# Kernel tuning notes

Measured on AMD Instinct MI355X. Metric: run time of the kernel, lower is better.

## Reference

```python
import jax, jax.numpy as jnp
import numpy as np

TOPK = 13
NUM_CLASSES = 80
ALPHA = 1.0
BETA = 6.0
EPS = 1e-9
B, N, IMG = 16, 100, 640


def _anchor_points():
    pts = []
    for s in (8, 16, 32):
        n = IMG // s
        xs = (jnp.arange(n, dtype=jnp.float32) + 0.5) * s
        gy, gx = jnp.meshgrid(xs, xs, indexing='ij')
        pts.append(jnp.stack([gx.reshape(-1), gy.reshape(-1)], axis=-1))
    return jnp.concatenate(pts, axis=0)  # [8400, 2]


def setup_inputs() -> dict:
    key = jax.random.key(0)
    k = jax.random.split(key, 6)
    anchor_points = _anchor_points()
    M = anchor_points.shape[0]
    pred_scores = jax.random.uniform(k[0], (B, M, NUM_CLASSES), dtype=jnp.float32)
    ctr = anchor_points[None] + jax.random.normal(k[1], (B, M, 2), dtype=jnp.float32) * 8.0
    wh = jax.random.uniform(k[2], (B, M, 2), minval=8.0, maxval=128.0, dtype=jnp.float32)
    pred_bboxes = jnp.concatenate([ctr - wh * 0.5, ctr + wh * 0.5], axis=-1)
    gctr = jax.random.uniform(k[3], (B, N, 2), minval=32.0, maxval=IMG - 32.0, dtype=jnp.float32)
    gwh = jax.random.uniform(k[4], (B, N, 2), minval=16.0, maxval=256.0, dtype=jnp.float32)
    gt_bboxes = jnp.concatenate([gctr - gwh * 0.5, gctr + gwh * 0.5], axis=-1)
    gt_labels = jax.random.randint(k[5], (B, N, 1), 0, NUM_CLASSES)
    # first 60 GTs valid per image
    mask_gt = (jnp.arange(N)[None, :, None] < 60).astype(jnp.float32) * jnp.ones((B, 1, 1), jnp.float32)
    return dict(pred_scores=pred_scores, pred_bboxes=pred_bboxes, anchor_points=anchor_points,
                gt_bboxes=gt_bboxes, gt_labels=gt_labels, mask_gt=mask_gt)


def _iou(gt, pr):
    # gt [B,N,4], pr [B,M,4] -> [B,N,M]
    gt = gt[:, :, None, :]
    pr = pr[:, None, :, :]
    lt = jnp.maximum(gt[..., :2], pr[..., :2])
    rb = jnp.minimum(gt[..., 2:], pr[..., 2:])
    wh = jnp.clip(rb - lt, 0.0)
    inter = wh[..., 0] * wh[..., 1]
    ag = (gt[..., 2] - gt[..., 0]) * (gt[..., 3] - gt[..., 1])
    ap = (pr[..., 2] - pr[..., 0]) * (pr[..., 3] - pr[..., 1])
    return jnp.clip(inter / (ag + ap - inter + EPS), 0.0)


def _forward(pred_scores, pred_bboxes, anchor_points, gt_bboxes, gt_labels, mask_gt):
    Bq, M, C = pred_scores.shape
    Nq = gt_bboxes.shape[1]
    lab = gt_labels[..., 0].astype(jnp.int32)  # [B,N]
    # gather class score of each GT's label at every anchor: [B,N,M]
    cls = jnp.take_along_axis(pred_scores.transpose(0, 2, 1), lab[:, :, None], axis=1)
    overlaps = _iou(gt_bboxes, pred_bboxes)                       # [B,N,M]
    align = (cls ** ALPHA) * (overlaps ** BETA)                   # [B,N,M]
    # anchor-center-in-gt mask
    ap = anchor_points[None, None, :, :]                          # [1,1,M,2]
    d = jnp.concatenate([ap - gt_bboxes[:, :, None, :2], gt_bboxes[:, :, None, 2:] - ap], axis=-1)
    in_gts = (jnp.min(d, axis=-1) > EPS).astype(align.dtype)      # [B,N,M]
    # top-k candidates per GT
    _, idx = jax.lax.top_k(align * in_gts, TOPK)                  # [B,N,K]
    tmask = jnp.broadcast_to(mask_gt.astype(bool), (Bq, Nq, TOPK))
    idx = jnp.where(tmask, idx, 0)
    bi = jnp.arange(Bq)[:, None, None]
    ni = jnp.arange(Nq)[None, :, None]
    cnt = jnp.zeros((Bq, Nq, M), align.dtype).at[bi, ni, idx].add(1.0)
    is_in_topk = jnp.where(cnt > 1, jnp.zeros_like(cnt), cnt)
    mask_pos = is_in_topk * in_gts * mask_gt                      # [B,N,M]
    # resolve anchors assigned to multiple GTs by highest IoU
    fg = mask_pos.sum(axis=-2)                                    # [B,M]
    multi = fg[:, None, :] > 1
    max_idx = jnp.argmax(overlaps, axis=1)                        # [B,M]
    is_max = (jnp.arange(Nq)[None, :, None] == max_idx[:, None, :]).astype(mask_pos.dtype)
    mask_pos = jnp.where(multi, is_max, mask_pos)
    fg = mask_pos.sum(axis=-2)
    tgt_idx = jnp.argmax(mask_pos, axis=-2)                       # [B,M]
    # assemble targets
    tl = jnp.take_along_axis(lab, tgt_idx, axis=1)                # [B,M]
    tb = jnp.take_along_axis(gt_bboxes, tgt_idx[..., None], axis=1)  # [B,M,4]
    tl = jnp.where(fg > 0, tl, NUM_CLASSES)                       # bg index for negatives
    ts = jax.nn.one_hot(tl, NUM_CLASSES + 1, dtype=pred_scores.dtype)[..., :NUM_CLASSES]
    # normalized align metric scaling
    am = align * mask_pos
    pa = am.max(axis=-1, keepdims=True)                           # [B,N,1]
    po = (overlaps * mask_pos).max(axis=-1, keepdims=True)        # [B,N,1]
    norm = (am * po / (pa + EPS)).max(axis=-2)[..., None]         # [B,M,1]
    ts = ts * norm
    return tl, tb, ts, fg > 0


def reference(pred_scores, pred_bboxes, anchor_points, gt_bboxes, gt_labels, mask_gt):
    return _forward(pred_scores, pred_bboxes, anchor_points, gt_bboxes, gt_labels, mask_gt)
```

## Files before the change

### kernel.cpp

```cpp
#include <hip/hip_runtime.h>

#define BB 16
#define NN 100
#define MM 8400
#define CC 80
#define TOPK 13
#define EPSF 1e-9f

#define OUT_TL 0
#define OUT_TB (BB*MM)
#define OUT_TS (OUT_TB + BB*MM*4)
#define OUT_FG (OUT_TS + BB*MM*CC)

__device__ __forceinline__ float iou_f(float gx1, float gy1, float gx2, float gy2,
                                       float px1, float py1, float px2, float py2) {
    float ltx = fmaxf(gx1, px1), lty = fmaxf(gy1, py1);
    float rbx = fminf(gx2, px2), rby = fminf(gy2, py2);
    float w = fmaxf(rbx - ltx, 0.0f), h = fmaxf(rby - lty, 0.0f);
    float inter = w * h;
    float ag  = (gx2 - gx1) * (gy2 - gy1);
    float ap_ = (px2 - px1) * (py2 - py1);
    float r = inter / (ag + ap_ - inter + EPSF);
    return fmaxf(r, 0.0f);
}

__global__ __launch_bounds__(256) void k_init(float* __restrict__ out,
                                              int* __restrict__ fg_cnt,
                                              int* __restrict__ sel_n,
                                              unsigned* __restrict__ pa,
                                              unsigned* __restrict__ po) {
    int i = blockIdx.x * blockDim.x + threadIdx.x;
    int stride = gridDim.x * blockDim.x;
    float4* ts4 = (float4*)(out + OUT_TS);
    const int nts4 = BB * MM * CC / 4;
    float4 z = make_float4(0.f, 0.f, 0.f, 0.f);
    for (int j = i; j < nts4; j += stride) ts4[j] = z;
    for (int j = i; j < BB * MM; j += stride) { fg_cnt[j] = 0; sel_n[j] = 0x7fffffff; }
    for (int j = i; j < BB * NN; j += stride) { pa[j] = 0u; po[j] = 0u; }
}

__global__ __launch_bounds__(256) void k_topk(const float* __restrict__ ps,
                                              const float* __restrict__ pb,
                                              const float* __restrict__ ap,
                                              const float* __restrict__ gtb,
                                              const int* __restrict__ lab,
                                              const float* __restrict__ mgt,
                                              int* __restrict__ fg_cnt,
                                              int* __restrict__ sel_n) {
    int row = blockIdx.x;
    int b = row / NN;
    int n = row - b * NN;
    int tid = threadIdx.x;

    __shared__ float swV[4];
    __shared__ int   swI[4];

    if (mgt[row] == 0.0f) return;

    float gx1 = gtb[row * 4 + 0], gy1 = gtb[row * 4 + 1];
    float gx2 = gtb[row * 4 + 2], gy2 = gtb[row * 4 + 3];
    int l = lab[row];
    const float* psb = ps + (size_t)b * MM * CC + l;
    const float* pbb = pb + (size_t)b * MM * 4;

    float v[33];
    unsigned long long insideMask = 0ull;
    float lmax = -1.0f; int lidx = MM;

#pragma unroll
    for (int j = 0; j < 33; ++j) {
        int m = tid + (j << 8);
        bool valid = (j < 32) || (tid < 208);
        int mc = valid ? m : (MM - 1);
        float ax = ap[2 * mc], ay = ap[2 * mc + 1];
        float dmin = fminf(fminf(ax - gx1, ay - gy1), fminf(gx2 - ax, gy2 - ay));
        bool inside = valid && (dmin > EPSF);
        float val = valid ? 0.0f : -1.0f;
        if (__any(inside)) {
            if (inside) {
                float4 p = *(const float4*)(pbb + (size_t)m * 4);
                float ov = iou_f(gx1, gy1, gx2, gy2, p.x, p.y, p.z, p.w);
                float cls = psb[(size_t)m * CC];
                float o2 = ov * ov;
                val = cls * (o2 * o2 * o2);
                insideMask |= (1ull << j);
            }
        }
        v[j] = val;
        if (val > lmax) { lmax = val; lidx = m; }
    }

    for (int it = 0; it < TOPK; ++it) {
        float bv = lmax; int bi = lidx;
#pragma unroll
        for (int off = 32; off > 0; off >>= 1) {
            float ov_ = __shfl_xor(bv, off, 64);
            int   oi_ = __shfl_xor(bi, off, 64);
            if (ov_ > bv || (ov_ == bv && oi_ < bi)) { bv = ov_; bi = oi_; }
        }
        int wave = tid >> 6;
        if ((tid & 63) == 0) { swV[wave] = bv; swI[wave] = bi; }
        __syncthreads();
        float gv = swV[0]; int gi = swI[0];
#pragma unroll
        for (int w = 1; w < 4; ++w) {
            float wv = swV[w]; int wi = swI[w];
            if (wv > gv || (wv == gv && wi < gi)) { gv = wv; gi = wi; }
        }
        __syncthreads();

        if ((gi & 255) == tid) {
            int j = gi >> 8;
            if ((insideMask >> j) & 1ull) {
                atomicAdd(&fg_cnt[b * MM + gi], 1);
                atomicMin(&sel_n[b * MM + gi], n);
            }
            lmax = -1.0f; lidx = MM;
#pragma unroll
            for (int jj = 0; jj < 33; ++jj) {
                float vv = (jj == j) ? -2.0f : v[jj];
                v[jj] = vv;
                int m = tid + (jj << 8);
                bool valid = (jj < 32) || (tid < 208);
                if (valid && vv > lmax) { lmax = vv; lidx = m; }
            }
        }
    }
}

__global__ __launch_bounds__(256) void k_resolve(const float* __restrict__ ps,
                                                 const float* __restrict__ pb,
                                                 const float* __restrict__ gtb,
                                                 const int* __restrict__ lab,
                                                 const int* __restrict__ fg_cnt,
                                                 const int* __restrict__ sel_n,
                                                 int* __restrict__ tgt,
                                                 float* __restrict__ a_val,
                                                 unsigned* __restrict__ pa,
                                                 unsigned* __restrict__ po) {
    const int bpb = (MM + 255) / 256;
    int b = blockIdx.x / bpb;
    int m = (blockIdx.x % bpb) * 256 + threadIdx.x;

    __shared__ float sG[NN * 4];
    for (int i = threadIdx.x; i < NN * 4; i += 256) sG[i] = gtb[b * NN * 4 + i];
    __syncthreads();
    if (m >= MM) return;

    int idx = b * MM + m;
    int c = fg_cnt[idx];
    int t = -1;
    float4 p = *(const float4*)(pb + ((size_t)b * MM + m) * 4);
    if (c == 1) {
        t = sel_n[idx];
    } else if (c > 1) {
        float best = -1.0f;
        for (int n = 0; n < NN; ++n) {
            float ov = iou_f(sG[n * 4], sG[n * 4 + 1], sG[n * 4 + 2], sG[n * 4 + 3],
                             p.x, p.y, p.z, p.w);
            if (ov > best) { best = ov; t = n; }
        }
    }
    tgt[idx] = t;
    float av = 0.0f;
    if (t >= 0) {
        float ov = iou_f(sG[t * 4], sG[t * 4 + 1], sG[t * 4 + 2], sG[t * 4 + 3],
                         p.x, p.y, p.z, p.w);
        float cls = ps[((size_t)b * MM + m) * CC + lab[b * NN + t]];
        float o2 = ov * ov;
        av = cls * (o2 * o2 * o2);
        atomicMax(&pa[b * NN + t], __float_as_uint(av));
        atomicMax(&po[b * NN + t], __float_as_uint(ov));
    }
    a_val[idx] = av;
}

__global__ __launch_bounds__(256) void k_final(const float* __restrict__ gtb,
                                               const int* __restrict__ lab,
                                               const int* __restrict__ tgt,
                                               const float* __restrict__ a_val,
                                               const unsigned* __restrict__ pa,
                                               const unsigned* __restrict__ po,
                                               float* __restrict__ out) {
    const int bpb = (MM + 255) / 256;
    int b = blockIdx.x / bpb;
    int m = (blockIdx.x % bpb) * 256 + threadIdx.x;
    if (m >= MM) return;

    int idx = b * MM + m;
    int t = tgt[idx];
    int fg = (t >= 0) ? 1 : 0;
    int tsrc = fg ? t : 0;

    float4 tb4 = *(const float4*)(gtb + ((size_t)b * NN + tsrc) * 4);
    out[OUT_TL + idx] = fg ? (float)lab[b * NN + t] : (float)CC;
    *(float4*)(out + OUT_TB + (size_t)idx * 4) = tb4;
    out[OUT_FG + idx] = fg ? 1.0f : 0.0f;
    if (fg) {
        float paf = __uint_as_float(pa[b * NN + t]);
        float pof = __uint_as_float(po[b * NN + t]);
        float norm = (a_val[idx] * pof) / (paf + EPSF);
        out[OUT_TS + (size_t)idx * CC + lab[b * NN + t]] = norm;
    }
}

extern "C" void kernel_launch(void* const* d_in, const int* in_sizes, int n_in,
                              void* d_out, int out_size, void* d_ws, size_t ws_size,
                              hipStream_t stream) {
    const float* ps  = (const float*)d_in[0];
    const float* pb  = (const float*)d_in[1];
    const float* ap  = (const float*)d_in[2];
    const float* gtb = (const float*)d_in[3];
    const int*   lab = (const int*)d_in[4];
    const float* mgt = (const float*)d_in[5];
    float* out = (float*)d_out;

    char* w = (char*)d_ws;
    int* fg_cnt  = (int*)w;        w += (size_t)BB * MM * 4;
    int* sel_n   = (int*)w;        w += (size_t)BB * MM * 4;
    int* tgt     = (int*)w;        w += (size_t)BB * MM * 4;
    float* a_val = (float*)w;      w += (size_t)BB * MM * 4;
    unsigned* pa = (unsigned*)w;   w += (size_t)BB * NN * 4;
    unsigned* po = (unsigned*)w;   w += (size_t)BB * NN * 4;

    const int bpb = (MM + 255) / 256;

    k_init<<<1024, 256, 0, stream>>>(out, fg_cnt, sel_n, pa, po);
    k_topk<<<BB * NN, 256, 0, stream>>>(ps, pb, ap, gtb, lab, mgt, fg_cnt, sel_n);
    k_resolve<<<BB * bpb, 256, 0, stream>>>(ps, pb, gtb, lab, fg_cnt, sel_n, tgt, a_val, pa, po);
    k_final<<<BB * bpb, 256, 0, stream>>>(gtb, lab, tgt, a_val, pa, po, out);
}
```

Measured before the change: 83.66 us.

## Compact positive candidates for top-k and fuse ts zeroing into final write

Replaces the 13-round block-wide argmax with ballot-compacted positive candidates in shared memory and a single-wave selection. Row-range culling skips anchor chunks outside the GT box, and anchor coordinates are computed analytically rather than loaded. The separate zero-fill of the large ts output is removed; k_final writes complete class rows with the norm value in place. A fixed candidate cap risks dropping candidates for very large boxes.

```diff
diff --git a/kernel.cpp b/kernel.cpp
--- a/kernel.cpp
+++ b/kernel.cpp
@@ -6,6 +6,7 @@
 #define CC 80
 #define TOPK 13
 #define EPSF 1e-9f
+#define CAP 1408
 
 #define OUT_TL 0
 #define OUT_TB (BB*MM)
@@ -24,24 +25,43 @@
     return fmaxf(r, 0.0f);
 }
 
-__global__ __launch_bounds__(256) void k_init(float* __restrict__ out,
-                                              int* __restrict__ fg_cnt,
+__device__ __forceinline__ void anchor_xy(int m, float& ax, float& ay) {
+    if (m < 6400) {
+        int r = (int)(__umulhi((unsigned)(m >> 4), 0xCCCCCCCDu) >> 2);
+        int c = m - r * 80;
+        ax = (c + 0.5f) * 8.0f;  ay = (r + 0.5f) * 8.0f;
+    } else if (m < 8000) {
+        int mm = m - 6400;
+        int r = (int)(__umulhi((unsigned)(mm >> 3), 0xCCCCCCCDu) >> 2);
+        int c = mm - r * 40;
+        ax = (c + 0.5f) * 16.0f; ay = (r + 0.5f) * 16.0f;
+    } else {
+        int mm = m - 8000;
+        int r = (int)(__umulhi((unsigned)(mm >> 2), 0xCCCCCCCDu) >> 2);
+        int c = mm - r * 20;
+        ax = (c + 0.5f) * 32.0f; ay = (r + 0.5f) * 32.0f;
+    }
+}
+
+__device__ __forceinline__ unsigned long long shflxor_u64(unsigned long long v, int off) {
+    unsigned lo = (unsigned)v, hi = (unsigned)(v >> 32);
+    lo = (unsigned)__shfl_xor((int)lo, off, 64);
+    hi = (unsigned)__shfl_xor((int)hi, off, 64);
+    return ((unsigned long long)hi << 32) | lo;
+}
+
+__global__ __launch_bounds__(256) void k_init(int* __restrict__ fg_cnt,
                                               int* __restrict__ sel_n,
                                               unsigned* __restrict__ pa,
                                               unsigned* __restrict__ po) {
     int i = blockIdx.x * blockDim.x + threadIdx.x;
     int stride = gridDim.x * blockDim.x;
-    float4* ts4 = (float4*)(out + OUT_TS);
-    const int nts4 = BB * MM * CC / 4;
-    float4 z = make_float4(0.f, 0.f, 0.f, 0.f);
-    for (int j = i; j < nts4; j += stride) ts4[j] = z;
     for (int j = i; j < BB * MM; j += stride) { fg_cnt[j] = 0; sel_n[j] = 0x7fffffff; }
     for (int j = i; j < BB * NN; j += stride) { pa[j] = 0u; po[j] = 0u; }
 }
 
 __global__ __launch_bounds__(256) void k_topk(const float* __restrict__ ps,
                                               const float* __restrict__ pb,
-                                              const float* __restrict__ ap,
                                               const float* __restrict__ gtb,
                                               const int* __restrict__ lab,
                                               const float* __restrict__ mgt,
@@ -51,11 +71,14 @@
     int b = row / NN;
     int n = row - b * NN;
     int tid = threadIdx.x;
-
-    __shared__ float swV[4];
-    __shared__ int   swI[4];
+    int lane = tid & 63;
+
+    __shared__ unsigned long long cand[CAP];
+    __shared__ int nPos;
 
     if (mgt[row] == 0.0f) return;
+    if (tid == 0) nPos = 0;
+    __syncthreads();
 
     float gx1 = gtb[row * 4 + 0], gy1 = gtb[row * 4 + 1];
     float gx2 = gtb[row * 4 + 2], gy2 = gtb[row * 4 + 3];
@@ -63,19 +86,20 @@
     const float* psb = ps + (size_t)b * MM * CC + l;
     const float* pbb = pb + (size_t)b * MM * 4;
 
-    float v[33];
-    unsigned long long insideMask = 0ull;
-    float lmax = -1.0f; int lidx = MM;
-
-#pragma unroll
+    int rlo = (int)floorf(gy1 * 0.125f) - 1;
+    int rhi = (int)floorf(gy2 * 0.125f) + 1;
+
     for (int j = 0; j < 33; ++j) {
+        if (j < 25) {
+            int r0 = (j * 256) / 80, r1 = (j * 256 + 255) / 80;
+            if (r1 < rlo || r0 > rhi) continue;
+        }
         int m = tid + (j << 8);
-        bool valid = (j < 32) || (tid < 208);
-        int mc = valid ? m : (MM - 1);
-        float ax = ap[2 * mc], ay = ap[2 * mc + 1];
+        bool valid = m < MM;
+        float ax, ay; anchor_xy(valid ? m : 0, ax, ay);
         float dmin = fminf(fminf(ax - gx1, ay - gy1), fminf(gx2 - ax, gy2 - ay));
         bool inside = valid && (dmin > EPSF);
-        float val = valid ? 0.0f : -1.0f;
+        float val = 0.0f;
         if (__any(inside)) {
             if (inside) {
                 float4 p = *(const float4*)(pbb + (size_t)m * 4);
@@ -83,48 +107,87 @@
                 float cls = psb[(size_t)m * CC];
                 float o2 = ov * ov;
                 val = cls * (o2 * o2 * o2);
-                insideMask |= (1ull << j);
-            }
-        }
-        v[j] = val;
-        if (val > lmax) { lmax = val; lidx = m; }
-    }
-
-    for (int it = 0; it < TOPK; ++it) {
-        float bv = lmax; int bi = lidx;
+            }
+        }
+        bool pos = inside && (val > 0.0f);
+        unsigned long long bal = __ballot(pos);
+        if (bal) {
+            int leader = __ffsll(bal) - 1;
+            int cnt = __popcll(bal);
+            int base = 0;
+            if (lane == leader) base = atomicAdd(&nPos, cnt);
+            base = __shfl(base, leader, 64);
+            if (pos) {
+                int off = __popcll(bal & ((1ull << lane) - 1ull));
+                int slot = base + off;
+                if (slot < CAP)
+                    cand[slot] = ((unsigned long long)__float_as_uint(val) << 32) |
+                                 (unsigned long long)(0xFFFFFFFFu - (unsigned)m);
+            }
+        }
+    }
+    __syncthreads();
+    if (tid >= 64) return;
+
+    int P = nPos;
+    if (P > CAP) P = CAP;
+
+    if (P <= TOPK) {
+        if (lane < P) {
+            unsigned long long k = cand[lane];
+            int m = (int)(0xFFFFFFFFu - (unsigned)(k & 0xFFFFFFFFu));
+            atomicAdd(&fg_cnt[b * MM + m], 1);
+            atomicMin(&sel_n[b * MM + m], n);
+        }
+    } else {
+        unsigned long long prev = ~0ull;
+        for (int it = 0; it < TOPK; ++it) {
+            unsigned long long best = 0ull;
+            for (int i = lane; i < P; i += 64) {
+                unsigned long long k = cand[i];
+                if (k < prev && k > best) best = k;
+            }
 #pragma unroll
-        for (int off = 32; off > 0; off >>= 1) {
-            float ov_ = __shfl_xor(bv, off, 64);
-            int   oi_ = __shfl_xor(bi, off, 64);
-            if (ov_ > bv || (ov_ == bv && oi_ < bi)) { bv = ov_; bi = oi_; }
-        }
-        int wave = tid >> 6;
-        if ((tid & 63) == 0) { swV[wave] = bv; swI[wave] = bi; }
-        __syncthreads();
-        float gv = swV[0]; int gi = swI[0];
-#pragma unroll
-        for (int w = 1; w < 4; ++w) {
-            float wv = swV[w]; int wi = swI[w];
-            if (wv > gv || (wv == gv && wi < gi)) { gv = wv; gi = wi; }
-        }
-        __syncthreads();
-
-        if ((gi & 255) == tid) {
-            int j = gi >> 8;
-            if ((insideMask >> j) & 1ull) {
-                atomicAdd(&fg_cnt[b * MM + gi], 1);
-                atomicMin(&sel_n[b * MM + gi], n);
-            }
-            lmax = -1.0f; lidx = MM;
-#pragma unroll
-            for (int jj = 0; jj < 33; ++jj) {
-                float vv = (jj == j) ? -2.0f : v[jj];
-                v[jj] = vv;
-                int m = tid + (jj << 8);
-                bool valid = (jj < 32) || (tid < 208);
-                if (valid && vv > lmax) { lmax = vv; lidx = m; }
-            }
-        }
+            for (int off = 32; off > 0; off >>= 1) {
+                unsigned long long o = shflxor_u64(best, off);
+                if (o > best) best = o;
+            }
+            if (lane == 0) {
+                int m = (int)(0xFFFFFFFFu - (unsigned)(best & 0xFFFFFFFFu));
+                atomicAdd(&fg_cnt[b * MM + m], 1);
+                atomicMin(&sel_n[b * MM + m], n);
+            }
+            prev = best;
+        }
+    }
+
+    int r = TOPK - P;
+    for (int base = 0; base < MM && r > 0; base += 64) {
+        int m = base + lane;
+        bool valid = m < MM;
+        float ax, ay; anchor_xy(valid ? m : 0, ax, ay);
+        float dmin = fminf(fminf(ax - gx1, ay - gy1), fminf(gx2 - ax, gy2 - ay));
+        bool inside = valid && (dmin > EPSF);
+        float val = 0.0f;
+        if (__any(inside)) {
+            if (inside) {
+                float4 p = *(const float4*)(pbb + (size_t)m * 4);
+                float ov = iou_f(gx1, gy1, gx2, gy2, p.x, p.y, p.z, p.w);
+                float cls = psb[(size_t)m * CC];
+                float o2 = ov * ov;
+                val = cls * (o2 * o2 * o2);
+            }
+        }
+        bool pos = inside && (val > 0.0f);
+        bool zero = valid && !pos;
+        unsigned long long mask = __ballot(zero);
+        int rank = __popcll(mask & ((1ull << lane) - 1ull));
+        if (zero && rank < r && inside) {
+            atomicAdd(&fg_cnt[b * MM + m], 1);
+            atomicMin(&sel_n[b * MM + m], n);
+        }
+        int tot = __popcll(mask);
+        r -= (tot < r ? tot : r);
     }
 }
 
@@ -184,23 +247,50 @@
                                                float* __restrict__ out) {
     const int bpb = (MM + 255) / 256;
     int b = blockIdx.x / bpb;
-    int m = (blockIdx.x % bpb) * 256 + threadIdx.x;
-    if (m >= MM) return;
-
-    int idx = b * MM + m;
-    int t = tgt[idx];
-    int fg = (t >= 0) ? 1 : 0;
-    int tsrc = fg ? t : 0;
-
-    float4 tb4 = *(const float4*)(gtb + ((size_t)b * NN + tsrc) * 4);
-    out[OUT_TL + idx] = fg ? (float)lab[b * NN + t] : (float)CC;
-    *(float4*)(out + OUT_TB + (size_t)idx * 4) = tb4;
-    out[OUT_FG + idx] = fg ? 1.0f : 0.0f;
-    if (fg) {
-        float paf = __uint_as_float(pa[b * NN + t]);
-        float pof = __uint_as_float(po[b * NN + t]);
-        float norm = (a_val[idx] * pof) / (paf + EPSF);
-        out[OUT_TS + (size_t)idx * CC + lab[b * NN + t]] = norm;
+    int mblk = (blockIdx.x % bpb) * 256;
+    int tid = threadIdx.x;
+    int m = mblk + tid;
+
+    __shared__ int   sLab[256];
+    __shared__ float sNorm[256];
+
+    int lb = -1; float nv = 0.0f;
+    if (m < MM) {
+        int idx = b * MM + m;
+        int t = tgt[idx];
+        int fg = (t >= 0) ? 1 : 0;
+        int tsrc = fg ? t : 0;
+        float4 tb4 = *(const float4*)(gtb + ((size_t)b * NN + tsrc) * 4);
+        out[OUT_TL + idx] = fg ? (float)lab[b * NN + t] : (float)CC;
+        *(float4*)(out + OUT_TB + (size_t)idx * 4) = tb4;
+        out[OUT_FG + idx] = fg ? 1.0f : 0.0f;
+        if (fg) {
+            lb = lab[b * NN + t];
+            float paf = __uint_as_float(pa[b * NN + t]);
+            float pof = __uint_as_float(po[b * NN + t]);
+            nv = (a_val[idx] * pof) / (paf + EPSF);
+        }
+    }
+    sLab[tid] = lb;
+    sNorm[tid] = nv;
+    __syncthreads();
+
+    int nAnch = MM - mblk; if (nAnch > 256) nAnch = 256;
+    int nQuad = nAnch * 20;
+    float4* tsq = (float4*)(out + OUT_TS) + ((size_t)b * MM + mblk) * 20;
+    for (int k = tid; k < nQuad; k += 256) {
+        unsigned u = (unsigned)(k >> 2);
+        int a = (int)((u * 52429u) >> 18);
+        int c4 = k - a * 20;
+        int albl = sLab[a];
+        float av = sNorm[a];
+        int base4 = c4 << 2;
+        float4 z;
+        z.x = (albl == base4 + 0) ? av : 0.0f;
+        z.y = (albl == base4 + 1) ? av : 0.0f;
+        z.z = (albl == base4 + 2) ? av : 0.0f;
+        z.w = (albl == base4 + 3) ? av : 0.0f;
+        tsq[k] = z;
     }
 }
 
@@ -209,7 +299,6 @@
                               hipStream_t stream) {
     const float* ps  = (const float*)d_in[0];
     const float* pb  = (const float*)d_in[1];
-    const float* ap  = (const float*)d_in[2];
     const float* gtb = (const float*)d_in[3];
     const int*   lab = (const int*)d_in[4];
     const float* mgt = (const float*)d_in[5];
@@ -225,8 +314,8 @@
 
     const int bpb = (MM + 255) / 256;
 
-    k_init<<<1024, 256, 0, stream>>>(out, fg_cnt, sel_n, pa, po);
-    k_topk<<<BB * NN, 256, 0, stream>>>(ps, pb, ap, gtb, lab, mgt, fg_cnt, sel_n);
+    k_init<<<256, 256, 0, stream>>>(fg_cnt, sel_n, pa, po);
+    k_topk<<<BB * NN, 256, 0, stream>>>(ps, pb, gtb, lab, mgt, fg_cnt, sel_n);
     k_resolve<<<BB * bpb, 256, 0, stream>>>(ps, pb, gtb, lab, fg_cnt, sel_n, tgt, a_val, pa, po);
     k_final<<<BB * bpb, 256, 0, stream>>>(gtb, lab, tgt, a_val, pa, po, out);
 }
```

Result: faster. 79.30 us (-5.2%).
